# Kernel optimization log

Measured on AMD Instinct MI355X. Metric: run time of the kernel, lower is better.

Reference implementation:

```python
import jax, jax.numpy as jnp
import numpy as np

V, E, H, D, C, L = 100000, 300, 512, 512, 20, 2048


def gru_cell(x, h, Wih, Whh, bih, bhh):
    # PyTorch GRUCell: gates packed as [r; z; n] along first axis of W (3H rows)
    gi = x @ Wih.T + bih  # [3H]
    gh = h @ Whh.T + bhh  # [3H]
    ir, iz, i_n = gi[:H], gi[H:2 * H], gi[2 * H:]
    hr, hz, h_n = gh[:H], gh[H:2 * H], gh[2 * H:]
    r = jax.nn.sigmoid(ir + hr)
    z = jax.nn.sigmoid(iz + hz)
    n = jnp.tanh(i_n + r * h_n)
    return (1.0 - z) * n + z * h


def setup_inputs() -> dict:
    key = jax.random.key(0)
    ks = jax.random.split(key, 15)
    g = lambda k, shape, sc: (jax.random.normal(k, shape, dtype=jnp.float32) * sc)
    return {
        "sequence": jax.random.randint(ks[0], (L,), 0, V),
        "emb": g(ks[1], (V, E), 0.1),
        "Wih_f": g(ks[2], (3 * H, E), 0.05),
        "Whh_f": g(ks[3], (3 * H, H), 0.05),
        "bih_f": g(ks[4], (3 * H,), 0.05),
        "bhh_f": g(ks[5], (3 * H,), 0.05),
        "Wih_b": g(ks[6], (3 * H, E), 0.05),
        "Whh_b": g(ks[7], (3 * H, H), 0.05),
        "bih_b": g(ks[8], (3 * H,), 0.05),
        "bhh_b": g(ks[9], (3 * H,), 0.05),
        "W1": g(ks[10], (D, 2 * H), 0.05),
        "b1": g(ks[11], (D,), 0.05),
        "W2": g(ks[12], (C, D), 0.05),
        "b2": g(ks[13], (C,), 0.05),
    }


def reference(sequence, emb, Wih_f, Whh_f, bih_f, bhh_f,
              Wih_b, Whh_b, bih_b, bhh_b, W1, b1, W2, b2):
    x = emb[sequence]  # [L, E] embedding lookup
    h0 = jnp.zeros((H,), dtype=emb.dtype)

    def step_f(h, xt):
        return gru_cell(xt, h, Wih_f, Whh_f, bih_f, bhh_f), None

    def step_b(h, xt):
        return gru_cell(xt, h, Wih_b, Whh_b, bih_b, bhh_b), None

    hf, _ = jax.lax.scan(step_f, h0, x)
    hb, _ = jax.lax.scan(step_b, h0, x[::-1])

    h = jnp.concatenate([hf, hb])[None, :]  # [1, 2H]
    hid = jax.nn.relu(h @ W1.T + b1)        # dropout is identity at eval
    logits = hid @ W2.T + b2                # [1, C]
    return jax.nn.softmax(logits, axis=-1)
```

## Files before the change

### kernel.cpp

```cpp
#include <hip/hip_runtime.h>
#include <math.h>

constexpr int SEQ_L = 2048;
constexpr int EDIM  = 300;
constexpr int NCLS  = 20;
constexpr unsigned SENT = 0xFFA5A5A5u;

typedef float f32x4 __attribute__((ext_vector_type(4)));

__global__ __launch_bounds__(256) void init_kernel(uint4* H) {
  const int NT = 513 * 256;
  int idx = blockIdx.x * blockDim.x + threadIdx.x;
  const uint4 z = {0u, 0u, 0u, 0u};
  const uint4 s = {SENT, SENT, SENT, SENT};
#pragma unroll
  for (int i = 0; i < 4; ++i) {
    int q = i * NT + idx;
    if (q < 524544) H[q] = (q < 256) ? z : s;
  }
}

__global__ __launch_bounds__(256) void gi_kernel(
    const int* __restrict__ seq, const float* __restrict__ emb,
    const float* __restrict__ Wih_f, const float* __restrict__ bih_f,
    const float* __restrict__ bhh_f,
    const float* __restrict__ Wih_b, const float* __restrict__ bih_b,
    const float* __restrict__ bhh_b,
    float* __restrict__ gi_f, float* __restrict__ gi_b) {
  const int d = blockIdx.y;
  const float* Wih = d ? Wih_b : Wih_f;
  const float* bih = d ? bih_b : bih_f;
  const float* bhh = d ? bhh_b : bhh_f;
  float* gi = d ? gi_b : gi_f;
  const int t0 = blockIdx.x * 8;
  const int tid = threadIdx.x;

  __shared__ float xs[8][304];

  for (int i = tid; i < 8 * 75; i += 256) {
    int tt = i / 75, u = i - tt * 75;
    int t = t0 + tt;
    int s = seq[d ? (SEQ_L - 1 - t) : t];
    const float4* p = reinterpret_cast<const float4*>(emb + (size_t)s * EDIM);
    float4 v = p[u];
    xs[tt][u * 4 + 0] = v.x; xs[tt][u * 4 + 1] = v.y;
    xs[tt][u * 4 + 2] = v.z; xs[tt][u * 4 + 3] = v.w;
  }
  __syncthreads();

  for (int rr = 0; rr < 6; ++rr) {
    int j = rr * 256 + tid;
    const float4* wrow = reinterpret_cast<const float4*>(Wih + (size_t)j * EDIM);
    float acc[8];
#pragma unroll
    for (int tt = 0; tt < 8; ++tt) acc[tt] = 0.0f;
    for (int q = 0; q < EDIM / 4; ++q) {
      float4 w = wrow[q];
#pragma unroll
      for (int tt = 0; tt < 8; ++tt)
        acc[tt] += w.x * xs[tt][4 * q] + w.y * xs[tt][4 * q + 1] +
                   w.z * xs[tt][4 * q + 2] + w.w * xs[tt][4 * q + 3];
    }
    float bb = bih[j] + (j < 1024 ? bhh[j] : 0.0f);
#pragma unroll
    for (int tt = 0; tt < 8; ++tt)
      gi[(size_t)(t0 + tt) * 1536 + j] = acc[tt] + bb;
  }
}

__global__ __launch_bounds__(512, 2) void rnn_kernel(
    const float* __restrict__ Whh_f, const float* __restrict__ bhh_f,
    const float* __restrict__ Whh_b, const float* __restrict__ bhh_b,
    const float* __restrict__ gi_f, const float* __restrict__ gi_b,
    float* Hbuf) {
  const int tid  = threadIdx.x;
  const int lane = tid & 63;
  const int w    = tid >> 6;
  const int blk  = blockIdx.x;
  const int dir  = blk >> 4;
  const int j0   = (blk & 15) * 32;

  const float* Whh = dir ? Whh_b : Whh_f;
  const float* bhh = dir ? bhh_b : bhh_f;
  const float* gi  = dir ? gi_b : gi_f;

  alignas(16) __shared__ float hsh[512];
  alignas(16) __shared__ float part[8][12][68];
  __shared__ float rsum[96];

  f32x4 Wv[24];
#pragma unroll
  for (int g = 0; g < 3; ++g)
#pragma unroll
    for (int jj = 0; jj < 4; ++jj) {
      const f32x4* rp = reinterpret_cast<const f32x4*>(
                            Whh + (size_t)(g * 512 + j0 + w * 4 + jj) * 512) +
                        lane * 2;
      Wv[(g * 4 + jj) * 2]     = rp[0];
      Wv[(g * 4 + jj) * 2 + 1] = rp[1];
    }

  const int jl = j0 + lane;
  float bhn = 0.0f;
  if (w == 0 && lane < 32) bhn = bhh[1024 + jl];
  float hprev = 0.0f;

  const int pollOff = dir * 512 + w * 64 + lane;

  for (int t = 0; t < SEQ_L; ++t) {
    float ir = 0.f, iz = 0.f, inn = 0.f;
    if (w == 0 && lane < 32) {
      const float* git = gi + (size_t)t * 1536;
      ir  = git[jl];
      iz  = git[512 + jl];
      inn = git[1024 + jl];
    }

    const float* hp = Hbuf + (size_t)t * 1024 + pollOff;
    float hvp;
    for (;;) {
      hvp = __hip_atomic_load(hp, __ATOMIC_RELAXED, __HIP_MEMORY_SCOPE_AGENT);
      if (__ballot(__float_as_uint(hvp) == SENT) == 0ull) break;
    }
    hsh[w * 64 + lane] = hvp;
    __syncthreads();

    const f32x4* hq = reinterpret_cast<const f32x4*>(&hsh[lane * 8]);
    f32x4 h0 = hq[0], h1 = hq[1];

    float s_[12];
#pragma unroll
    for (int r = 0; r < 12; ++r) {
      f32x4 w0 = Wv[2 * r], w1 = Wv[2 * r + 1];
      s_[r] = w0.x * h0.x + w0.y * h0.y + w0.z * h0.z + w0.w * h0.w +
              w1.x * h1.x + w1.y * h1.y + w1.z * h1.z + w1.w * h1.w;
    }

#pragma unroll
    for (int r = 0; r < 12; ++r) part[w][r][lane] = s_[r];
    __builtin_amdgcn_wave_barrier();
    if (lane < 12) {
      const f32x4* rowp = reinterpret_cast<const f32x4*>(&part[w][lane][0]);
      f32x4 a4 = rowp[0];
#pragma unroll
      for (int q = 1; q < 16; ++q) a4 += rowp[q];
      rsum[w * 12 + lane] = (a4.x + a4.y) + (a4.z + a4.w);
    }
    __syncthreads();

    if (w == 0 && lane < 32) {
      int ww = lane >> 2, jj = lane & 3;
      float sr = rsum[ww * 12 + jj];
      float sz = rsum[ww * 12 + 4 + jj];
      float sn = rsum[ww * 12 + 8 + jj];
      float rr = 1.0f / (1.0f + __expf(-(ir + sr)));
      float zz = 1.0f / (1.0f + __expf(-(iz + sz)));
      float nn = tanhf(inn + rr * (sn + bhn));
      float hnew = (1.0f - zz) * nn + zz * hprev;
      hprev = hnew;
      __hip_atomic_store(Hbuf + (size_t)(t + 1) * 1024 + dir * 512 + jl, hnew,
                         __ATOMIC_RELAXED, __HIP_MEMORY_SCOPE_AGENT);
    }
  }
}

__global__ __launch_bounds__(1024) void cls_kernel(
    const float* __restrict__ Hfin,
    const float* __restrict__ W1, const float* __restrict__ b1,
    const float* __restrict__ W2, const float* __restrict__ b2,
    float* __restrict__ out) {
  __shared__ float hcat[1024];
  __shared__ float hid[512];
  __shared__ float logits[NCLS];
  const int tid = threadIdx.x;
  hcat[tid] = Hfin[tid];
  __syncthreads();

  const int lane = tid & 63, widx = tid >> 6;
  for (int rr = 0; rr < 32; ++rr) {
    int row = widx * 32 + rr;
    const float4* wrow = reinterpret_cast<const float4*>(W1 + (size_t)row * 1024);
    float acc = 0.0f;
#pragma unroll
    for (int c = 0; c < 4; ++c) {
      int k = c * 256 + lane * 4;
      float4 v = wrow[c * 64 + lane];
      acc += v.x * hcat[k] + v.y * hcat[k + 1] + v.z * hcat[k + 2] +
             v.w * hcat[k + 3];
    }
#pragma unroll
    for (int mask = 32; mask >= 1; mask >>= 1) acc += __shfl_xor(acc, mask, 64);
    if (lane == 0) hid[row] = fmaxf(acc + b1[row], 0.0f);
  }
  __syncthreads();

  if (tid < NCLS) {
    const float4* wrow = reinterpret_cast<const float4*>(W2 + (size_t)tid * 512);
    float acc = 0.0f;
    for (int q = 0; q < 128; ++q) {
      float4 v = wrow[q];
      int k = q * 4;
      acc += v.x * hid[k] + v.y * hid[k + 1] + v.z * hid[k + 2] +
             v.w * hid[k + 3];
    }
    logits[tid] = acc + b2[tid];
  }
  __syncthreads();

  if (tid == 0) {
    float m = -1e30f;
    for (int i = 0; i < NCLS; ++i) m = fmaxf(m, logits[i]);
    float s = 0.0f;
    float e[NCLS];
    for (int i = 0; i < NCLS; ++i) { e[i] = __expf(logits[i] - m); s += e[i]; }
    float inv = 1.0f / s;
    for (int i = 0; i < NCLS; ++i) out[i] = e[i] * inv;
  }
}

extern "C" void kernel_launch(void* const* d_in, const int* in_sizes, int n_in,
                              void* d_out, int out_size, void* d_ws,
                              size_t ws_size, hipStream_t stream) {
  (void)in_sizes; (void)n_in; (void)out_size; (void)ws_size;
  const int*   seq   = (const int*)d_in[0];
  const float* emb   = (const float*)d_in[1];
  const float* Wih_f = (const float*)d_in[2];
  const float* Whh_f = (const float*)d_in[3];
  const float* bih_f = (const float*)d_in[4];
  const float* bhh_f = (const float*)d_in[5];
  const float* Wih_b = (const float*)d_in[6];
  const float* Whh_b = (const float*)d_in[7];
  const float* bih_b = (const float*)d_in[8];
  const float* bhh_b = (const float*)d_in[9];
  const float* W1    = (const float*)d_in[10];
  const float* b1    = (const float*)d_in[11];
  const float* W2    = (const float*)d_in[12];
  const float* b2    = (const float*)d_in[13];
  float* out = (float*)d_out;

  float* gi_f = (float*)d_ws;
  float* gi_b = gi_f + (size_t)SEQ_L * 1536;
  float* Hbuf = gi_b + (size_t)SEQ_L * 1536;

  hipLaunchKernelGGL(init_kernel, dim3(513), dim3(256), 0, stream,
                     (uint4*)Hbuf);
  hipLaunchKernelGGL(gi_kernel, dim3(SEQ_L / 8, 2), dim3(256), 0, stream,
                     seq, emb, Wih_f, bih_f, bhh_f, Wih_b, bih_b, bhh_b,
                     gi_f, gi_b);
  hipLaunchKernelGGL(rnn_kernel, dim3(32), dim3(512), 0, stream,
                     Whh_f, bhh_f, Whh_b, bhh_b, gi_f, gi_b, Hbuf);
  hipLaunchKernelGGL(cls_kernel, dim3(1), dim3(1024), 0, stream,
                     Hbuf + (size_t)SEQ_L * 1024, W1, b1, W2, b2, out);
}
```

Baseline: 4.111 ms.

## Compute gate outputs per wave and double-buffer hidden state to drop barrier

Each wave now finishes the GRU gate math for its own 4 hidden units. It gathers the r/z/n partial sums and input-gate values with lane shuffles, instead of writing them to shared memory and having wave 0 compute all 32 units after a second block-wide barrier. The shared hidden-state buffer is double-buffered by timestep parity so the removed barrier does not create a read/write race. This removes one __syncthreads per timestep from the serial critical path, at the cost of more lanes doing redundant reduction work and more global stores issued per block.

```diff
diff --git a/kernel.cpp b/kernel.cpp
--- a/kernel.cpp
+++ b/kernel.cpp
@@ -79,14 +79,14 @@
   const int blk  = blockIdx.x;
   const int dir  = blk >> 4;
   const int j0   = (blk & 15) * 32;
+  const int jw   = j0 + w * 4;
 
   const float* Whh = dir ? Whh_b : Whh_f;
   const float* bhh = dir ? bhh_b : bhh_f;
   const float* gi  = dir ? gi_b : gi_f;
 
-  alignas(16) __shared__ float hsh[512];
+  alignas(16) __shared__ float hsh[2][512];
   alignas(16) __shared__ float part[8][12][68];
-  __shared__ float rsum[96];
 
   f32x4 Wv[24];
 #pragma unroll
@@ -94,27 +94,25 @@
 #pragma unroll
     for (int jj = 0; jj < 4; ++jj) {
       const f32x4* rp = reinterpret_cast<const f32x4*>(
-                            Whh + (size_t)(g * 512 + j0 + w * 4 + jj) * 512) +
+                            Whh + (size_t)(g * 512 + jw + jj) * 512) +
                         lane * 2;
       Wv[(g * 4 + jj) * 2]     = rp[0];
       Wv[(g * 4 + jj) * 2 + 1] = rp[1];
     }
 
-  const int jl = j0 + lane;
+  const int jj = lane & 3;
   float bhn = 0.0f;
-  if (w == 0 && lane < 32) bhn = bhh[1024 + jl];
+  if (lane < 4) bhn = bhh[1024 + jw + lane];
   float hprev = 0.0f;
 
   const int pollOff = dir * 512 + w * 64 + lane;
 
   for (int t = 0; t < SEQ_L; ++t) {
-    float ir = 0.f, iz = 0.f, inn = 0.f;
-    if (w == 0 && lane < 32) {
-      const float* git = gi + (size_t)t * 1536;
-      ir  = git[jl];
-      iz  = git[512 + jl];
-      inn = git[1024 + jl];
-    }
+    const int p = t & 1;
+
+    float giv = 0.0f;
+    if (lane < 12)
+      giv = gi[(size_t)t * 1536 + (lane >> 2) * 512 + jw + jj];
 
     const float* hp = Hbuf + (size_t)t * 1024 + pollOff;
     float hvp;
@@ -122,10 +120,10 @@
       hvp = __hip_atomic_load(hp, __ATOMIC_RELAXED, __HIP_MEMORY_SCOPE_AGENT);
       if (__ballot(__float_as_uint(hvp) == SENT) == 0ull) break;
     }
-    hsh[w * 64 + lane] = hvp;
+    hsh[p][w * 64 + lane] = hvp;
     __syncthreads();
 
-    const f32x4* hq = reinterpret_cast<const f32x4*>(&hsh[lane * 8]);
+    const f32x4* hq = reinterpret_cast<const f32x4*>(&hsh[p][lane * 8]);
     f32x4 h0 = hq[0], h1 = hq[1];
 
     float s_[12];
@@ -139,27 +137,29 @@
 #pragma unroll
     for (int r = 0; r < 12; ++r) part[w][r][lane] = s_[r];
     __builtin_amdgcn_wave_barrier();
-    if (lane < 12) {
-      const f32x4* rowp = reinterpret_cast<const f32x4*>(&part[w][lane][0]);
+    float sv = 0.0f;
+    {
+      int r = lane < 12 ? lane : 0;
+      const f32x4* rowp = reinterpret_cast<const f32x4*>(&part[w][r][0]);
       f32x4 a4 = rowp[0];
 #pragma unroll
       for (int q = 1; q < 16; ++q) a4 += rowp[q];
-      rsum[w * 12 + lane] = (a4.x + a4.y) + (a4.z + a4.w);
-    }
-    __syncthreads();
-
-    if (w == 0 && lane < 32) {
-      int ww = lane >> 2, jj = lane & 3;
-      float sr = rsum[ww * 12 + jj];
-      float sz = rsum[ww * 12 + 4 + jj];
-      float sn = rsum[ww * 12 + 8 + jj];
-      float rr = 1.0f / (1.0f + __expf(-(ir + sr)));
-      float zz = 1.0f / (1.0f + __expf(-(iz + sz)));
-      float nn = tanhf(inn + rr * (sn + bhn));
+      sv = (a4.x + a4.y) + (a4.z + a4.w);
+    }
+
+    float s_z = __shfl(sv, 4 + jj, 64);
+    float g_z = __shfl(giv, 4 + jj, 64);
+    float s_n = __shfl(sv, 8 + jj, 64);
+    float g_n = __shfl(giv, 8 + jj, 64);
+
+    if (lane < 4) {
+      float rr = 1.0f / (1.0f + __expf(-(giv + sv)));
+      float zz = 1.0f / (1.0f + __expf(-(g_z + s_z)));
+      float nn = tanhf(g_n + rr * (s_n + bhn));
       float hnew = (1.0f - zz) * nn + zz * hprev;
       hprev = hnew;
-      __hip_atomic_store(Hbuf + (size_t)(t + 1) * 1024 + dir * 512 + jl, hnew,
-                         __ATOMIC_RELAXED, __HIP_MEMORY_SCOPE_AGENT);
+      __hip_atomic_store(Hbuf + (size_t)(t + 1) * 1024 + dir * 512 + jw + lane,
+                         hnew, __ATOMIC_RELAXED, __HIP_MEMORY_SCOPE_AGENT);
     }
   }
 }
```

Result: slower. 4.997 ms (+21.5%).
